# Optimization experiments

Measured on AMD Instinct MI355X. Metric: run time of the kernel, lower is better.

The kernel has to match this reference:

```python
import jax, jax.numpy as jnp
import numpy as np

D = 256      # input_dim
SE = 512     # emo seq len
SC = 512     # cause seq len
CKS = 8      # chunksize
KC = 3       # causes per emo utterance


def _linear(k, fi, fo):
    kw, kb = jax.random.split(k)
    bound = 1.0 / np.sqrt(fi)
    w = jax.random.uniform(kw, (fi, fo), jnp.float32, -bound, bound)
    b = jax.random.uniform(kb, (fo,), jnp.float32, -bound, bound)
    return w, b


def setup_inputs() -> dict:
    key = jax.random.key(0)
    ks = jax.random.split(key, 12)
    text_emo = jax.random.normal(ks[0], (SE, 1, D), jnp.float32)
    text_cau = jax.random.normal(ks[1], (SC, 1, D), jnp.float32)
    label_ck = jnp.ones((SE, SC // CKS), jnp.int64 if jax.config.jax_enable_x64 else jnp.int32)
    label3 = jax.random.randint(ks[2], (SE, 1, KC), 0, SC)
    rep_W, rep_b = _linear(ks[3], D, D)
    W_W, W_b = _linear(ks[4], 2 * D, D)
    Wo_W, Wo_b = _linear(ks[5], D, 2)
    # GRU params, torch layout transposed to (in, 3*hidden); gate order r,z,n
    bound = 1.0 / np.sqrt(D)
    gru_Wih = jax.random.uniform(ks[6], (D, 3 * D), jnp.float32, -bound, bound)
    gru_Whh = jax.random.uniform(ks[7], (D, 3 * D), jnp.float32, -bound, bound)
    gru_bih = jax.random.uniform(ks[8], (3 * D,), jnp.float32, -bound, bound)
    gru_bhh = jax.random.uniform(ks[9], (3 * D,), jnp.float32, -bound, bound)
    W3_W, W3_b = _linear(ks[10], 3 * D + 1, D)
    cls_W, cls_b = _linear(ks[11], D, 2)
    return {"text_emo": text_emo, "text_cau": text_cau, "label_ck": label_ck,
            "label3": label3, "chunksize": CKS,
            "rep_W": rep_W, "rep_b": rep_b, "W_W": W_W, "W_b": W_b,
            "Wo_W": Wo_W, "Wo_b": Wo_b,
            "gru_Wih": gru_Wih, "gru_Whh": gru_Whh,
            "gru_bih": gru_bih, "gru_bhh": gru_bhh,
            "W3_W": W3_W, "W3_b": W3_b, "cls_W": cls_W, "cls_b": cls_b}


def reference(text_emo, text_cau, label_ck, label3, chunksize,
              rep_W, rep_b, W_W, W_b, Wo_W, Wo_b,
              gru_Wih, gru_Whh, gru_bih, gru_bhh,
              W3_W, W3_b, cls_W, cls_b):
    d = text_emo.shape[-1]
    # shared representation: relu(Linear)
    te = jax.nn.relu(text_emo @ rep_W + rep_b)   # (SE,1,d)
    tc = jax.nn.relu(text_cau @ rep_W + rep_b)   # (SC,1,d)
    emo = te[:, 0, :]                             # (SE,d) batch==1
    cau = tc[:, 0, :]                             # (SC,d)
    se, sc = emo.shape[0], cau.shape[0]
    C = sc // chunksize
    chunks = cau.reshape(C, chunksize, d)         # torch.split of text_cau

    # GRU over each chunk with zero initial state; take last hidden.
    # (Original re-runs this identically for every emo timestep; math is the same.)
    def gru_last(ch):
        def step(h, x):
            gx = x @ gru_Wih + gru_bih
            gh = h @ gru_Whh + gru_bhh
            xr, xz, xn = jnp.split(gx, 3)
            hr, hz, hn = jnp.split(gh, 3)
            r = jax.nn.sigmoid(xr + hr)
            z = jax.nn.sigmoid(xz + hz)
            n = jnp.tanh(xn + r * hn)
            return (1.0 - z) * n + z * h, None
        h, _ = jax.lax.scan(step, jnp.zeros((d,), ch.dtype), ch)
        return h
    ch_last = jax.vmap(gru_last)(chunks)          # (C,d)

    # phase 2: chunk-level classifier per emo timestep (dropout = identity, eval)
    chunkEmb = jnp.concatenate([
        jnp.broadcast_to(emo[:, None, :], (se, C, d)),
        jnp.broadcast_to(ch_last[None, :, :], (se, C, d))], axis=-1)  # (SE,C,2d)
    hidden = jax.nn.sigmoid(chunkEmb @ W_W + W_b)
    phase2 = jax.nn.log_softmax(hidden @ Wo_W + Wo_b, axis=-1)        # (SE,C,2)

    # phase 3: t_ratio=1 -> idx = label_ck[j]; label_ck all ones selects every
    # chunk, so utt_c == full text_cau for each emo step.
    item2 = jnp.linalg.norm(emo[:, None, :] - cau[None, :, :], axis=-1, keepdims=True)
    delta = jnp.concatenate([
        jnp.broadcast_to(emo[:, None, :], (se, sc, d)),
        jnp.broadcast_to(cau[None, :, :], (se, sc, d)),
        item2,
        emo[:, None, :] * cau[None, :, :]], axis=-1)   # (SE,SC,3d+1)
    h3 = jax.nn.relu(delta @ W3_W + W3_b)
    p = jax.nn.log_softmax(h3 @ cls_W + cls_b, axis=-1)               # (SE,SC,2)

    # label3_out: per emo step, binary cause vector over cause utterances
    lab3 = label3[:, 0, :]                                            # (SE,KC)
    L_cau = jnp.zeros((se, sc), phase2.dtype).at[
        jnp.arange(se)[:, None], lab3].set(1.0)
    return phase2, p, L_cau
```

## Files before the change

### kernel.cpp

```cpp
#include <hip/hip_runtime.h>
#include <hip/hip_bf16.h>
#include <hip/hip_fp16.h>
#include <math.h>

#define D   256
#define SE  512
#define SC  512
#define CKS 8
#define NC  64
#define KC  3

typedef __attribute__((ext_vector_type(8))) short short8_t;
typedef __attribute__((ext_vector_type(4))) short short4_t;
typedef __attribute__((ext_vector_type(4))) float f32x4;

__device__ __forceinline__ float sigmoidf_(float x) { return 1.f / (1.f + __expf(-x)); }
__device__ __forceinline__ short bf16s(float f) {
    union { __hip_bfloat16 h; short s; } u; u.h = __float2bfloat16(f); return u.s;
}
__device__ __forceinline__ float bflo(unsigned int u) {
    union { unsigned int u; float f; } v; v.u = u << 16; return v.f;
}
__device__ __forceinline__ float bfhi(unsigned int u) {
    union { unsigned int u; float f; } v; v.u = u & 0xffff0000u; return v.f;
}
#define GLOAD_LDS16(g, l) \
    __builtin_amdgcn_global_load_lds((const __attribute__((address_space(1))) void*)(g), \
                                     (__attribute__((address_space(3))) void*)(l), 16, 0, 0)

__global__ __launch_bounds__(256) void prep_all_kernel(
    const float* __restrict__ W3, const float* __restrict__ Wih,
    const float* __restrict__ Whh, const float* __restrict__ WW,
    const float* __restrict__ repW, const float* __restrict__ clsW,
    short* __restrict__ Bprep, uint2* __restrict__ Wih16, uint2* __restrict__ Whh16,
    float4* __restrict__ WWq, float4* __restrict__ W3q,
    float4* __restrict__ repWq, unsigned int* __restrict__ clsP)
{
    const int b = blockIdx.x, t = threadIdx.x;
    if (b < 32) {
        const int idx = b * 256 + t;
        const int p = idx >> 11, k = (idx >> 3) & 255, G = idx & 7;
        const int dbase = p * 64 + ((G ^ (k & 7)) << 3);
        #pragma unroll
        for (int e = 0; e < 8; ++e)
            Bprep[idx * 8 + e] = bf16s(W3[(size_t)(513 + dbase + e) * D + k]);
    } else if (b < 416) {
        const bool ih = (b < 224);
        const int tid = (b - (ih ? 32 : 224)) * 256 + t;
        const float* W = ih ? Wih : Whh;
        const int base = (tid / 768) * 4 * 768 + (tid % 768);
        float f0 = W[base], f1 = W[base + 768], f2 = W[base + 1536], f3 = W[base + 2304];
        __half2 plo = __halves2half2(__float2half_rn(f0), __float2half_rn(f1));
        __half2 phi = __halves2half2(__float2half_rn(f2), __float2half_rn(f3));
        uint2 o; o.x = *(unsigned int*)&plo; o.y = *(unsigned int*)&phi;
        (ih ? Wih16 : Whh16)[tid] = o;
    } else if (b < 672) {
        const bool ww = (b < 544);
        const int tid = (b - (ww ? 416 : 544)) * 256 + t;
        const int h = tid >> 14, rem = tid & 16383, d4 = rem >> 8, k = rem & 255;
        const float* src = (ww ? WW : W3) + (size_t)(h * 256 + 4 * d4) * D + k;
        (ww ? WWq : W3q)[tid] = make_float4(src[0], src[256], src[512], src[768]);
    } else if (b < 736) {
        const int tid = (b - 672) * 256 + t;
        const int d4 = tid >> 8, k = tid & 255;
        const float* src = repW + (size_t)(4 * d4) * D + k;
        repWq[tid] = make_float4(src[0], src[256], src[512], src[768]);
    } else {
        unsigned int c0 = (unsigned int)(unsigned short)bf16s(clsW[t * 2]);
        unsigned int c1 = (unsigned int)(unsigned short)bf16s(clsW[t * 2 + 1]);
        clsP[t] = c0 | (c1 << 16);
    }
}

__global__ __launch_bounds__(256) void rep4_kernel(
    const float* __restrict__ te, const float* __restrict__ tc,
    const float4* __restrict__ repWq, const float* __restrict__ b,
    float* __restrict__ emo, float* __restrict__ cau,
    short* __restrict__ emoB, short* __restrict__ cauB)
{
    const int r0 = blockIdx.x * 4, t = threadIdx.x;
    const float* X = (r0 < SE) ? (te + (size_t)r0 * D) : (tc + (size_t)(r0 - SE) * D);
    __shared__ __align__(16) float xs[4][D];
    #pragma unroll
    for (int r = 0; r < 4; ++r) xs[r][t] = X[r * D + t];
    __syncthreads();
    float acc0 = 0.f, acc1 = 0.f, acc2 = 0.f, acc3 = 0.f;
    #pragma unroll 8
    for (int q = 0; q < 64; ++q) {
        float4 w = repWq[q * 256 + t];
        float4 x0 = *(const float4*)&xs[0][q * 4];
        float4 x1 = *(const float4*)&xs[1][q * 4];
        float4 x2 = *(const float4*)&xs[2][q * 4];
        float4 x3 = *(const float4*)&xs[3][q * 4];
        acc0 = fmaf(x0.x, w.x, acc0); acc0 = fmaf(x0.y, w.y, acc0); acc0 = fmaf(x0.z, w.z, acc0); acc0 = fmaf(x0.w, w.w, acc0);
        acc1 = fmaf(x1.x, w.x, acc1); acc1 = fmaf(x1.y, w.y, acc1); acc1 = fmaf(x1.z, w.z, acc1); acc1 = fmaf(x1.w, w.w, acc1);
        acc2 = fmaf(x2.x, w.x, acc2); acc2 = fmaf(x2.y, w.y, acc2); acc2 = fmaf(x2.z, w.z, acc2); acc2 = fmaf(x2.w, w.w, acc2);
        acc3 = fmaf(x3.x, w.x, acc3); acc3 = fmaf(x3.y, w.y, acc3); acc3 = fmaf(x3.z, w.z, acc3); acc3 = fmaf(x3.w, w.w, acc3);
    }
    const float bb = b[t];
    float v[4] = {fmaxf(acc0 + bb, 0.f), fmaxf(acc1 + bb, 0.f), fmaxf(acc2 + bb, 0.f), fmaxf(acc3 + bb, 0.f)};
    #pragma unroll
    for (int r = 0; r < 4; ++r) {
        const int row = r0 + r;
        if (row < SE) { emo[(size_t)row * D + t] = v[r]; emoB[(size_t)row * D + t] = bf16s(v[r]); }
        else { cau[(size_t)(row - SE) * D + t] = v[r]; cauB[(size_t)(row - SE) * D + t] = bf16s(v[r]); }
    }
}

__global__ __launch_bounds__(768) void gx2_kernel(
    const float* __restrict__ cau, const uint2* __restrict__ Wih16,
    const float* __restrict__ bih, __half* __restrict__ GX16)
{
    const int r0 = blockIdx.x * 2, t = threadIdx.x;
    __shared__ uint2 xs4[2][64];
    if (t < 128) {
        const int r = t >> 6, c = t & 63;
        float4 v = *(const float4*)&cau[(size_t)(r0 + r) * D + c * 4];
        __half2 plo = __halves2half2(__float2half_rn(v.x), __float2half_rn(v.y));
        __half2 phi = __halves2half2(__float2half_rn(v.z), __float2half_rn(v.w));
        uint2 o; o.x = *(unsigned int*)&plo; o.y = *(unsigned int*)&phi;
        xs4[r][c] = o;
    }
    __syncthreads();
    __half2 a00 = __float2half2_rn(0.f), a01 = __float2half2_rn(0.f);
    __half2 a10 = __float2half2_rn(0.f), a11 = __float2half2_rn(0.f);
    #pragma unroll 8
    for (int q = 0; q < 64; ++q) {
        uint2 w = Wih16[q * 768 + t];
        uint2 x0 = xs4[0][q], x1 = xs4[1][q];
        a00 = __hfma2(*(__half2*)&w.x, *(__half2*)&x0.x, a00);
        a01 = __hfma2(*(__half2*)&w.y, *(__half2*)&x0.y, a01);
        a10 = __hfma2(*(__half2*)&w.x, *(__half2*)&x1.x, a10);
        a11 = __hfma2(*(__half2*)&w.y, *(__half2*)&x1.y, a11);
    }
    const float bi = bih[t];
    float g0 = bi + __low2float(a00) + __high2float(a00) + __low2float(a01) + __high2float(a01);
    float g1 = bi + __low2float(a10) + __high2float(a10) + __low2float(a11) + __high2float(a11);
    GX16[(size_t)r0 * 768 + t] = __float2half_rn(g0);
    GX16[(size_t)(r0 + 1) * 768 + t] = __float2half_rn(g1);
}

__global__ __launch_bounds__(768) void gru_rec_kernel(
    const __half* __restrict__ GX16, const uint2* __restrict__ Whh16,
    const float* __restrict__ bhh, float* __restrict__ ch_last)
{
    const int c = blockIdx.x, t = threadIdx.x;
    __shared__ uint2 hqu[64];
    __shared__ float gh_s[768];
    uint2 wreg[64];
    #pragma unroll
    for (int q = 0; q < 64; ++q) wreg[q] = Whh16[q * 768 + t];
    float h = 0.f;
    if (t < 64) { uint2 z; z.x = 0u; z.y = 0u; hqu[t] = z; }
    __syncthreads();
    const float bh = bhh[t];
    for (int s = 0; s < CKS; ++s) {
        const int row = c * CKS + s;
        __half2 a0 = __float2half2_rn(0.f), a1 = __float2half2_rn(0.f);
        #pragma unroll
        for (int q = 0; q < 64; ++q) {
            uint2 hv = hqu[q];
            a0 = __hfma2(*(__half2*)&wreg[q].x, *(__half2*)&hv.x, a0);
            a1 = __hfma2(*(__half2*)&wreg[q].y, *(__half2*)&hv.y, a1);
        }
        gh_s[t] = bh + __low2float(a0) + __high2float(a0) + __low2float(a1) + __high2float(a1);
        __syncthreads();
        if (t < 256) {
            const float gxr = __half2float(GX16[(size_t)row * 768 + t]);
            const float gxz = __half2float(GX16[(size_t)row * 768 + 256 + t]);
            const float gxn = __half2float(GX16[(size_t)row * 768 + 512 + t]);
            float r = sigmoidf_(gxr + gh_s[t]);
            float z = sigmoidf_(gxz + gh_s[256 + t]);
            float n = tanhf(gxn + r * gh_s[512 + t]);
            h = (1.f - z) * n + z * h;
            float f1 = __shfl_down(h, 1);
            float f2 = __shfl_down(h, 2);
            float f3 = __shfl_down(h, 3);
            if ((t & 3) == 0) {
                __half2 plo = __halves2half2(__float2half_rn(h),  __float2half_rn(f1));
                __half2 phi = __halves2half2(__float2half_rn(f2), __float2half_rn(f3));
                uint2 o; o.x = *(unsigned int*)&plo; o.y = *(unsigned int*)&phi;
                hqu[t >> 2] = o;
            }
        }
        __syncthreads();
    }
    if (t < 256) ch_last[c * D + t] = h;
}

__global__ __launch_bounds__(256) void dual_all4_kernel(
    const float* __restrict__ emo, const float* __restrict__ cau, const float* __restrict__ chl,
    const float4* __restrict__ WWq, const float4* __restrict__ W3q,
    const float* __restrict__ Wb, const float* __restrict__ W3b,
    float* __restrict__ HE, float* __restrict__ HC, float* __restrict__ Ae,
    short* __restrict__ AcB)
{
    const int r0 = blockIdx.x * 4, t = threadIdx.x;
    const float* X; const float4* Wq; float bias;
    int seg;
    if (r0 < 512)       { X = emo + (size_t)r0 * D;          Wq = WWq;         bias = 0.f;    seg = 0; }
    else if (r0 < 576)  { X = chl + (size_t)(r0 - 512) * D;  Wq = WWq + 16384; bias = Wb[t];  seg = 1; }
    else if (r0 < 1088) { X = emo + (size_t)(r0 - 576) * D;  Wq = W3q;         bias = 0.f;    seg = 2; }
    else                { X = cau + (size_t)(r0 - 1088) * D; Wq = W3q + 16384; bias = W3b[t]; seg = 3; }
    __shared__ __align__(16) float xs[4][D];
    #pragma unroll
    for (int r = 0; r < 4; ++r) xs[r][t] = X[r * D + t];
    __syncthreads();
    float a0 = bias, a1 = bias, a2 = bias, a3 = bias;
    #pragma unroll 8
    for (int q = 0; q < 64; ++q) {
        float4 w = Wq[q * 256 + t];
        float4 x0 = *(const float4*)&xs[0][q * 4];
        float4 x1 = *(const float4*)&xs[1][q * 4];
        float4 x2 = *(const float4*)&xs[2][q * 4];
        float4 x3 = *(const float4*)&xs[3][q * 4];
        a0 = fmaf(x0.x, w.x, a0); a0 = fmaf(x0.y, w.y, a0); a0 = fmaf(x0.z, w.z, a0); a0 = fmaf(x0.w, w.w, a0);
        a1 = fmaf(x1.x, w.x, a1); a1 = fmaf(x1.y, w.y, a1); a1 = fmaf(x1.z, w.z, a1); a1 = fmaf(x1.w, w.w, a1);
        a2 = fmaf(x2.x, w.x, a2); a2 = fmaf(x2.y, w.y, a2); a2 = fmaf(x2.z, w.z, a2); a2 = fmaf(x2.w, w.w, a2);
        a3 = fmaf(x3.x, w.x, a3); a3 = fmaf(x3.y, w.y, a3); a3 = fmaf(x3.z, w.z, a3); a3 = fmaf(x3.w, w.w, a3);
    }
    float av[4] = {a0, a1, a2, a3};
    #pragma unroll
    for (int r = 0; r < 4; ++r) {
        const int row = r0 + r;
        if (seg == 0)      HE[(size_t)row * D + t] = av[r];
        else if (seg == 1) HC[(size_t)(row - 512) * D + t] = av[r];
        else if (seg == 2) Ae[(size_t)(row - 576) * D + t] = av[r];
        else               AcB[(size_t)(row - 1088) * D + t] = bf16s(av[r]);
    }
}

__global__ __launch_bounds__(256) void phase2_kernel(
    const float* __restrict__ HE, const float* __restrict__ HC,
    const float* __restrict__ WoW, const float* __restrict__ Wob,
    float* __restrict__ out)
{
    const int i = blockIdx.x, t = threadIdx.x;
    const int c = t >> 2, sub = t & 3;
    __shared__ __align__(16) float he_s[D];
    he_s[t] = HE[(size_t)i * D + t];
    __syncthreads();
    float v0 = 0.f, v1 = 0.f;
    const float* hcRow = HC + (size_t)c * D;
    #pragma unroll 4
    for (int kk = 0; kk < 16; ++kk) {
        const int k4 = sub * 64 + kk * 4;
        float4 he = *(const float4*)&he_s[k4];
        float4 hc = *(const float4*)&hcRow[k4];
        float hk;
        hk = sigmoidf_(he.x + hc.x); { float2 wo = *(const float2*)&WoW[(k4 + 0) * 2]; v0 = fmaf(hk, wo.x, v0); v1 = fmaf(hk, wo.y, v1); }
        hk = sigmoidf_(he.y + hc.y); { float2 wo = *(const float2*)&WoW[(k4 + 1) * 2]; v0 = fmaf(hk, wo.x, v0); v1 = fmaf(hk, wo.y, v1); }
        hk = sigmoidf_(he.z + hc.z); { float2 wo = *(const float2*)&WoW[(k4 + 2) * 2]; v0 = fmaf(hk, wo.x, v0); v1 = fmaf(hk, wo.y, v1); }
        hk = sigmoidf_(he.w + hc.w); { float2 wo = *(const float2*)&WoW[(k4 + 3) * 2]; v0 = fmaf(hk, wo.x, v0); v1 = fmaf(hk, wo.y, v1); }
    }
    v0 += __shfl_xor(v0, 1); v0 += __shfl_xor(v0, 2);
    v1 += __shfl_xor(v1, 1); v1 += __shfl_xor(v1, 2);
    if (sub == 0) {
        float l0 = v0 + Wob[0], l1 = v1 + Wob[1];
        float m = fmaxf(l0, l1);
        float lse = m + __logf(__expf(l0 - m) + __expf(l1 - m));
        float2 o; o.x = l0 - lse; o.y = l1 - lse;
        *(float2*)&out[((size_t)i * NC + c) * 2] = o;
    }
}

__global__ __launch_bounds__(512) void p_kernel(
    const short* __restrict__ emoB, const short* __restrict__ cauB,
    const float* __restrict__ Ae,  const short* __restrict__ AcB,
    const float* __restrict__ wn,  const short* __restrict__ Bprep,
    const float* __restrict__ clsW,
    float* __restrict__ pp)
{
    const int t = threadIdx.x;
    const int i0 = blockIdx.x * 8;
    const int jt = blockIdx.y >> 1, kh = blockIdx.y & 1;
    const int j0 = jt * 64;
    const int l = t & 63, wave = t >> 6;
    const int hi = l >> 4, lo = l & 15;
    const int wj = wave >> 1, wk = wave & 1;
    const int j_base = wj * 16, k_base = wk * 64;

    __shared__ __align__(16) short B_s[32768];
    __shared__ __align__(16) short A_s[4096];
    __shared__ float it2_s[64];
    __shared__ float part2[64][2][2];

    #pragma unroll
    for (int r = 0; r < 8; ++r) {
        const int g = r * 512 + t;
        const int p = g >> 10, rem = g & 1023;
        GLOAD_LDS16(Bprep + ((size_t)(p * 256 + kh * 128) * 8 + rem) * 8, &B_s[g * 8]);
    }

    const int jlb = t >> 4;
    const int dl = (t & 15) * 4;
    const int g_w = dl >> 3, half_w = (dl >> 2) & 1;
    int addrA[2];
    #pragma unroll
    for (int r = 0; r < 2; ++r)
        addrA[r] = (r * 32 + jlb) * 64 + ((g_w ^ (jlb & 7)) << 3) + half_w * 4;

    int kcol[4]; float wn_r[4], c0_r[4], c1_r[4];
    #pragma unroll
    for (int kf = 0; kf < 4; ++kf) {
        const int kg = kh * 128 + k_base + kf * 16 + lo;
        kcol[kf] = kg;
        wn_r[kf] = wn[kg];
        c0_r[kf] = clsW[kg * 2]; c1_r[kf] = clsW[kg * 2 + 1];
    }
    const int swzf0 = (hi ^ (lo & 7)) << 3;
    const int swzf1 = ((4 + hi) ^ (lo & 7)) << 3;
    __syncthreads();

    for (int ii = 0; ii < 8; ++ii) {
        const int i = i0 + ii;
        f32x4 acc[4];
        #pragma unroll
        for (int kf = 0; kf < 4; ++kf) acc[kf] = (f32x4)(0.f);
        float dist[2] = {0.f, 0.f};

        for (int p = 0; p < 4; ++p) {
            const uint2 eu = *(const uint2*)&emoB[(size_t)i * D + p * 64 + dl];
            const float e0 = bflo(eu.x), e1 = bfhi(eu.x), e2 = bflo(eu.y), e3 = bfhi(eu.y);
            __syncthreads();
            #pragma unroll
            for (int r = 0; r < 2; ++r) {
                volatile const unsigned int* cp =
                    (volatile const unsigned int*)&cauB[(size_t)(j0 + r * 32 + jlb) * D + p * 64 + dl];
                const unsigned int cux = cp[0];
                const unsigned int cuy = cp[1];
                const float c0 = bflo(cux), c1 = bfhi(cux), c2 = bflo(cuy), c3 = bfhi(cuy);
                float dv = dist[r];
                float d0 = e0 - c0; dv = fmaf(d0, d0, dv);
                float d1 = e1 - c1; dv = fmaf(d1, d1, dv);
                float d2 = e2 - c2; dv = fmaf(d2, d2, dv);
                float d3 = e3 - c3; dv = fmaf(d3, d3, dv);
                dist[r] = dv;
                short4_t av;
                av.x = bf16s(c0 * e0); av.y = bf16s(c1 * e1);
                av.z = bf16s(c2 * e2); av.w = bf16s(c3 * e3);
                *(short4_t*)&A_s[addrA[r]] = av;
            }
            __syncthreads();
            #pragma unroll
            for (int df = 0; df < 2; ++df) {
                const int swz = df ? swzf1 : swzf0;
                const short8_t a = *(const short8_t*)&A_s[(j_base + lo) * 64 + swz];
                short8_t b[4];
                #pragma unroll
                for (int kf = 0; kf < 4; ++kf)
                    b[kf] = *(const short8_t*)&B_s[p * 8192 + (k_base + kf * 16 + lo) * 64 + swz];
                #pragma unroll
                for (int kf = 0; kf < 4; ++kf)
                    acc[kf] = __builtin_amdgcn_mfma_f32_16x16x32_bf16(a, b[kf], acc[kf], 0, 0, 0);
            }
        }

        #pragma unroll
        for (int r = 0; r < 2; ++r) {
            float v = dist[r];
            v += __shfl_xor(v, 1); v += __shfl_xor(v, 2);
            v += __shfl_xor(v, 4); v += __shfl_xor(v, 8);
            if (lo == 0) it2_s[r * 32 + jlb] = sqrtf(v);
        }
        __syncthreads();

        float Ae_r[4];
        #pragma unroll
        for (int kf = 0; kf < 4; ++kf) Ae_r[kf] = Ae[(size_t)i * D + kcol[kf]];
        #pragma unroll
        for (int q = 0; q < 4; ++q) {
            const int j = j_base + hi * 4 + q;
            const float it2v = it2_s[j];
            const short* AcRow = AcB + (size_t)(j0 + j) * D;
            float sv0 = 0.f, sv1 = 0.f;
            #pragma unroll
            for (int kf = 0; kf < 4; ++kf) {
                float s = acc[kf][q] + Ae_r[kf]
                        + bflo((unsigned int)(unsigned short)AcRow[kcol[kf]])
                        + it2v * wn_r[kf];
                float h = fmaxf(s, 0.f);
                sv0 = fmaf(h, c0_r[kf], sv0); sv1 = fmaf(h, c1_r[kf], sv1);
            }
            sv0 += __shfl_xor(sv0, 1); sv0 += __shfl_xor(sv0, 2);
            sv0 += __shfl_xor(sv0, 4); sv0 += __shfl_xor(sv0, 8);
            sv1 += __shfl_xor(sv1, 1); sv1 += __shfl_xor(sv1, 2);
            sv1 += __shfl_xor(sv1, 4); sv1 += __shfl_xor(sv1, 8);
            if (lo == 0) { part2[j][wk][0] = sv0; part2[j][wk][1] = sv1; }
        }
        __syncthreads();
        if (t < 64) {
            float2 o;
            o.x = part2[t][0][0] + part2[t][1][0];
            o.y = part2[t][0][1] + part2[t][1][1];
            *(float2*)&pp[(((size_t)kh * SE + i) * SC + j0 + t) * 2] = o;
        }
    }
}

__global__ __launch_bounds__(512) void pfin_kernel(
    const float* __restrict__ pp, const float* __restrict__ clsb,
    float* __restrict__ pout)
{
    const int i = blockIdx.x, j = threadIdx.x;
    const float2 a = *(const float2*)&pp[((size_t)i * SC + j) * 2];
    const float2 b = *(const float2*)&pp[(((size_t)SE + i) * SC + j) * 2];
    float s0 = a.x + b.x + clsb[0];
    float s1 = a.y + b.y + clsb[1];
    float m = fmaxf(s0, s1);
    float lse = m + __logf(__expf(s0 - m) + __expf(s1 - m));
    float2 o; o.x = s0 - lse; o.y = s1 - lse;
    *(float2*)&pout[((size_t)i * SC + j) * 2] = o;
}

__global__ __launch_bounds__(128) void lcau_kernel(const int* __restrict__ label3, float* __restrict__ L)
{
    const int row = blockIdx.x, t = threadIdx.x;
    float4 z; z.x = z.y = z.z = z.w = 0.f;
    *(float4*)&L[(size_t)row * SC + t * 4] = z;
    __syncthreads();
    if (t < KC) {
        int j = label3[row * KC + t];
        L[(size_t)row * SC + j] = 1.0f;
    }
}

extern "C" void kernel_launch(void* const* d_in, const int* in_sizes, int n_in,
                              void* d_out, int out_size, void* d_ws, size_t ws_size,
                              hipStream_t stream)
{
    const float* text_emo = (const float*)d_in[0];
    const float* text_cau = (const float*)d_in[1];
    const int*   label3   = (const int*)d_in[3];
    const float* rep_W = (const float*)d_in[5];
    const float* rep_b = (const float*)d_in[6];
    const float* W_W   = (const float*)d_in[7];
    const float* W_b   = (const float*)d_in[8];
    const float* Wo_W  = (const float*)d_in[9];
    const float* Wo_b  = (const float*)d_in[10];
    const float* gWih  = (const float*)d_in[11];
    const float* gWhh  = (const float*)d_in[12];
    const float* gbih  = (const float*)d_in[13];
    const float* gbhh  = (const float*)d_in[14];
    const float* W3_W  = (const float*)d_in[15];
    const float* W3_b  = (const float*)d_in[16];
    const float* cls_W = (const float*)d_in[17];
    const float* cls_b = (const float*)d_in[18];

    float* out        = (float*)d_out;
    float* phase2_out = out;
    float* p_out      = out + SE * NC * 2;
    float* lcau_out   = out + SE * NC * 2 + SE * SC * 2;

    float* ws  = (float*)d_ws;
    float* emo = ws;
    float* cau = emo + 131072;
    float* chl = cau + 131072;
    float* HE  = chl + 16384;
    float* HC  = HE + 131072;
    float* Ae  = HC + 16384;
    float4* WWq = (float4*)(Ae + 131072);
    float4* W3q = WWq + 32768;
    short* AcB   = (short*)(W3q + 32768);
    short* Bprep = AcB + 131072;
    uint2* Wih16 = (uint2*)(Bprep + 65536);
    uint2* Whh16 = Wih16 + 49152;
    float4* repWq = (float4*)(Whh16 + 49152);
    short* cauB = (short*)(repWq + 16384);
    short* emoB = cauB + 131072;
    unsigned int* clsP = (unsigned int*)(emoB + 131072);
    float* pp = (float*)(clsP + 256);
    __half* GX16 = (__half*)HE;

    prep_all_kernel<<<737, 256, 0, stream>>>(W3_W, gWih, gWhh, W_W, rep_W, cls_W,
                                             Bprep, Wih16, Whh16, WWq, W3q, repWq, clsP);
    rep4_kernel<<<256, 256, 0, stream>>>(text_emo, text_cau, repWq, rep_b, emo, cau, emoB, cauB);
    gx2_kernel<<<256, 768, 0, stream>>>(cau, Wih16, gbih, GX16);
    gru_rec_kernel<<<NC, 768, 0, stream>>>(GX16, Whh16, gbhh, chl);
    dual_all4_kernel<<<400, 256, 0, stream>>>(emo, cau, chl, WWq, W3q, W_b, W3_b,
                                              HE, HC, Ae, AcB);
    phase2_kernel<<<SE, 256, 0, stream>>>(HE, HC, Wo_W, Wo_b, phase2_out);
    p_kernel<<<dim3(64, 16), 512, 0, stream>>>(emoB, cauB, Ae, AcB, W3_W + 512 * D,
                                               Bprep, cls_W, pp);
    pfin_kernel<<<SE, 512, 0, stream>>>(pp, cls_b, p_out);
    lcau_kernel<<<SE, 128, 0, stream>>>(label3, lcau_out);
}
```

Measured before the change: 186.2 us.

## Build MFMA A-fragments in registers from a transposed cause copy

rep4 now also writes a bf16 copy of cau in a chunk-transposed layout (8-element groups by row), so each lane in p_kernel can load the 8 cause values that match its own MFMA A-fragment. The emo*cau product is formed directly in registers and fed to the MFMA, which removes the shared-memory A staging buffer and the two block barriers per k-slice. The distance reduction now uses cross-lane shuffles instead of a shared array, and one barrier is added at the end of each row iteration. The cost is an extra global write in rep4 and a larger workspace. The cause loads in p_kernel are also less coalesced per lane.

```diff
diff --git a/kernel.cpp b/kernel.cpp
--- a/kernel.cpp
+++ b/kernel.cpp
@@ -76,7 +76,8 @@
     const float* __restrict__ te, const float* __restrict__ tc,
     const float4* __restrict__ repWq, const float* __restrict__ b,
     float* __restrict__ emo, float* __restrict__ cau,
-    short* __restrict__ emoB, short* __restrict__ cauB)
+    short* __restrict__ emoB, short* __restrict__ cauB,
+    short* __restrict__ cauT)
 {
     const int r0 = blockIdx.x * 4, t = threadIdx.x;
     const float* X = (r0 < SE) ? (te + (size_t)r0 * D) : (tc + (size_t)(r0 - SE) * D);
@@ -102,8 +103,14 @@
     #pragma unroll
     for (int r = 0; r < 4; ++r) {
         const int row = r0 + r;
-        if (row < SE) { emo[(size_t)row * D + t] = v[r]; emoB[(size_t)row * D + t] = bf16s(v[r]); }
-        else { cau[(size_t)(row - SE) * D + t] = v[r]; cauB[(size_t)(row - SE) * D + t] = bf16s(v[r]); }
+        const short bv = bf16s(v[r]);
+        if (row < SE) { emo[(size_t)row * D + t] = v[r]; emoB[(size_t)row * D + t] = bv; }
+        else {
+            const int jr = row - SE;
+            cau[(size_t)jr * D + t] = v[r];
+            cauB[(size_t)jr * D + t] = bv;
+            cauT[(((size_t)(t >> 3)) * 512 + jr) * 8 + (t & 7)] = bv;
+        }
     }
 }
 
@@ -265,7 +272,7 @@
 }
 
 __global__ __launch_bounds__(512) void p_kernel(
-    const short* __restrict__ emoB, const short* __restrict__ cauB,
+    const short* __restrict__ emoB, const short* __restrict__ cauT,
     const float* __restrict__ Ae,  const short* __restrict__ AcB,
     const float* __restrict__ wn,  const short* __restrict__ Bprep,
     const float* __restrict__ clsW,
@@ -279,10 +286,9 @@
     const int hi = l >> 4, lo = l & 15;
     const int wj = wave >> 1, wk = wave & 1;
     const int j_base = wj * 16, k_base = wk * 64;
+    const int myj = j0 + j_base + lo;
 
     __shared__ __align__(16) short B_s[32768];
-    __shared__ __align__(16) short A_s[4096];
-    __shared__ float it2_s[64];
     __shared__ float part2[64][2][2];
 
     #pragma unroll
@@ -291,14 +297,6 @@
         const int p = g >> 10, rem = g & 1023;
         GLOAD_LDS16(Bprep + ((size_t)(p * 256 + kh * 128) * 8 + rem) * 8, &B_s[g * 8]);
     }
-
-    const int jlb = t >> 4;
-    const int dl = (t & 15) * 4;
-    const int g_w = dl >> 3, half_w = (dl >> 2) & 1;
-    int addrA[2];
-    #pragma unroll
-    for (int r = 0; r < 2; ++r)
-        addrA[r] = (r * 32 + jlb) * 64 + ((g_w ^ (jlb & 7)) << 3) + half_w * 4;
 
     int kcol[4]; float wn_r[4], c0_r[4], c1_r[4];
     #pragma unroll
@@ -317,53 +315,48 @@
         f32x4 acc[4];
         #pragma unroll
         for (int kf = 0; kf < 4; ++kf) acc[kf] = (f32x4)(0.f);
-        float dist[2] = {0.f, 0.f};
-
+        float dist = 0.f;
+
+        #pragma unroll
         for (int p = 0; p < 4; ++p) {
-            const uint2 eu = *(const uint2*)&emoB[(size_t)i * D + p * 64 + dl];
-            const float e0 = bflo(eu.x), e1 = bfhi(eu.x), e2 = bflo(eu.y), e3 = bfhi(eu.y);
-            __syncthreads();
             #pragma unroll
-            for (int r = 0; r < 2; ++r) {
+            for (int df = 0; df < 2; ++df) {
+                const int dg = p * 8 + df * 4 + hi;
+                const uint4 eu = *(const uint4*)&emoB[(size_t)i * D + dg * 8];
+                const float e0 = bflo(eu.x), e1 = bfhi(eu.x), e2 = bflo(eu.y), e3 = bfhi(eu.y);
+                const float e4 = bflo(eu.z), e5 = bfhi(eu.z), e6 = bflo(eu.w), e7 = bfhi(eu.w);
                 volatile const unsigned int* cp =
-                    (volatile const unsigned int*)&cauB[(size_t)(j0 + r * 32 + jlb) * D + p * 64 + dl];
-                const unsigned int cux = cp[0];
-                const unsigned int cuy = cp[1];
-                const float c0 = bflo(cux), c1 = bfhi(cux), c2 = bflo(cuy), c3 = bfhi(cuy);
-                float dv = dist[r];
+                    (volatile const unsigned int*)&cauT[((size_t)dg * 512 + myj) * 8];
+                const unsigned int u0 = cp[0], u1 = cp[1], u2 = cp[2], u3 = cp[3];
+                const float c0 = bflo(u0), c1 = bfhi(u0), c2 = bflo(u1), c3 = bfhi(u1);
+                const float c4 = bflo(u2), c5 = bfhi(u2), c6 = bflo(u3), c7 = bfhi(u3);
+                float dv = dist;
                 float d0 = e0 - c0; dv = fmaf(d0, d0, dv);
                 float d1 = e1 - c1; dv = fmaf(d1, d1, dv);
                 float d2 = e2 - c2; dv = fmaf(d2, d2, dv);
                 float d3 = e3 - c3; dv = fmaf(d3, d3, dv);
-                dist[r] = dv;
-                short4_t av;
-                av.x = bf16s(c0 * e0); av.y = bf16s(c1 * e1);
-                av.z = bf16s(c2 * e2); av.w = bf16s(c3 * e3);
-                *(short4_t*)&A_s[addrA[r]] = av;
+                float d4 = e4 - c4; dv = fmaf(d4, d4, dv);
+                float d5 = e5 - c5; dv = fmaf(d5, d5, dv);
+                float d6 = e6 - c6; dv = fmaf(d6, d6, dv);
+                float d7 = e7 - c7; dv = fmaf(d7, d7, dv);
+                dist = dv;
+                short8_t af;
+                af[0] = bf16s(c0 * e0); af[1] = bf16s(c1 * e1);
+                af[2] = bf16s(c2 * e2); af[3] = bf16s(c3 * e3);
+                af[4] = bf16s(c4 * e4); af[5] = bf16s(c5 * e5);
+                af[6] = bf16s(c6 * e6); af[7] = bf16s(c7 * e7);
+                const int swz = df ? swzf1 : swzf0;
+                #pragma unroll
+                for (int kf = 0; kf < 4; ++kf) {
+                    const short8_t bf = *(volatile const short8_t*)&B_s[p * 8192 + (k_base + kf * 16 + lo) * 64 + swz];
+                    acc[kf] = __builtin_amdgcn_mfma_f32_16x16x32_bf16(af, bf, acc[kf], 0, 0, 0);
+                }
             }
-            __syncthreads();
-            #pragma unroll
-            for (int df = 0; df < 2; ++df) {
-                const int swz = df ? swzf1 : swzf0;
-                const short8_t a = *(const short8_t*)&A_s[(j_base + lo) * 64 + swz];
-                short8_t b[4];
-                #pragma unroll
-                for (int kf = 0; kf < 4; ++kf)
-                    b[kf] = *(const short8_t*)&B_s[p * 8192 + (k_base + kf * 16 + lo) * 64 + swz];
-                #pragma unroll
-                for (int kf = 0; kf < 4; ++kf)
-                    acc[kf] = __builtin_amdgcn_mfma_f32_16x16x32_bf16(a, b[kf], acc[kf], 0, 0, 0);
-            }
-        }
-
-        #pragma unroll
-        for (int r = 0; r < 2; ++r) {
-            float v = dist[r];
-            v += __shfl_xor(v, 1); v += __shfl_xor(v, 2);
-            v += __shfl_xor(v, 4); v += __shfl_xor(v, 8);
-            if (lo == 0) it2_s[r * 32 + jlb] = sqrtf(v);
-        }
-        __syncthreads();
+        }
+
+        float dv = dist;
+        dv += __shfl_xor(dv, 16); dv += __shfl_xor(dv, 32);
+        const float itv_all = sqrtf(dv);
 
         float Ae_r[4];
         #pragma unroll
@@ -371,14 +364,14 @@
         #pragma unroll
         for (int q = 0; q < 4; ++q) {
             const int j = j_base + hi * 4 + q;
-            const float it2v = it2_s[j];
+            const float itv = __shfl(itv_all, j - j_base + (wj & 0) );
             const short* AcRow = AcB + (size_t)(j0 + j) * D;
             float sv0 = 0.f, sv1 = 0.f;
             #pragma unroll
             for (int kf = 0; kf < 4; ++kf) {
                 float s = acc[kf][q] + Ae_r[kf]
                         + bflo((unsigned int)(unsigned short)AcRow[kcol[kf]])
-                        + it2v * wn_r[kf];
+                        + itv * wn_r[kf];
                 float h = fmaxf(s, 0.f);
                 sv0 = fmaf(h, c0_r[kf], sv0); sv1 = fmaf(h, c1_r[kf], sv1);
             }
@@ -395,6 +388,7 @@
             o.y = part2[t][0][1] + part2[t][1][1];
             *(float2*)&pp[(((size_t)kh * SE + i) * SC + j0 + t) * 2] = o;
         }
+        __syncthreads();
     }
 }
 
@@ -470,17 +464,18 @@
     short* emoB = cauB + 131072;
     unsigned int* clsP = (unsigned int*)(emoB + 131072);
     float* pp = (float*)(clsP + 256);
+    short* cauT = (short*)(pp + 1048576);
     __half* GX16 = (__half*)HE;
 
     prep_all_kernel<<<737, 256, 0, stream>>>(W3_W, gWih, gWhh, W_W, rep_W, cls_W,
                                              Bprep, Wih16, Whh16, WWq, W3q, repWq, clsP);
-    rep4_kernel<<<256, 256, 0, stream>>>(text_emo, text_cau, repWq, rep_b, emo, cau, emoB, cauB);
+    rep4_kernel<<<256, 256, 0, stream>>>(text_emo, text_cau, repWq, rep_b, emo, cau, emoB, cauB, cauT);
     gx2_kernel<<<256, 768, 0, stream>>>(cau, Wih16, gbih, GX16);
     gru_rec_kernel<<<NC, 768, 0, stream>>>(GX16, Whh16, gbhh, chl);
     dual_all4_kernel<<<400, 256, 0, stream>>>(emo, cau, chl, WWq, W3q, W_b, W3_b,
                                               HE, HC, Ae, AcB);
     phase2_kernel<<<SE, 256, 0, stream>>>(HE, HC, Wo_W, Wo_b, phase2_out);
-    p_kernel<<<dim3(64, 16), 512, 0, stream>>>(emoB, cauB, Ae, AcB, W3_W + 512 * D,
+    p_kernel<<<dim3(64, 16), 512, 0, stream>>>(emoB, cauT, Ae, AcB, W3_W + 512 * D,
                                                Bprep, cls_W, pp);
     pfin_kernel<<<SE, 512, 0, stream>>>(pp, cls_b, p_out);
     lcau_kernel<<<SE, 128, 0, stream>>>(label3, lcau_out);
```

Result: slower. 339.4 us (+82.3%).
